# Kernel tuning notes

Hardware: AMD Instinct MI355X
Metric: run time of the kernel (lower is better)

## Reference

```python
import jax, jax.numpy as jnp
import numpy as np

B, S, D = 2, 2048, 2048
HQ, HKV, HD = 16, 8, 128
F = 8192
V = 32000
L = 2
SW = 512
SOFTCAP = 50.0
THETA = 10000.0
EPS = 1e-6
LAYER_TYPES = ("sliding_attention", "full_attention")
SCALE = HD ** -0.5


def _rms_norm(x, w):
    # Gemma-style RMSNorm: fp32 compute, (1 + weight) scale
    x32 = x.astype(jnp.float32)
    n = x32 * jax.lax.rsqrt(jnp.mean(x32 * x32, axis=-1, keepdims=True) + EPS)
    return (n * (1.0 + w.astype(jnp.float32))).astype(x.dtype)


def _rotate_half(x):
    x1, x2 = jnp.split(x, 2, axis=-1)
    return jnp.concatenate([-x2, x1], axis=-1)


def _rope_cos_sin(position_ids):
    inv_freq = 1.0 / (THETA ** (jnp.arange(0, HD, 2, dtype=jnp.float32) / HD))  # [HD/2]
    freqs = position_ids.astype(jnp.float32)[..., None] * inv_freq  # [B,S,HD/2]
    emb = jnp.concatenate([freqs, freqs], axis=-1)  # [B,S,HD]
    return jnp.cos(emb), jnp.sin(emb)


def _apply_rope(q, k, cos, sin):
    # q,k: [B,H,S,HD]; cos,sin: [B,S,HD] -> unsqueeze head dim
    c, s = cos[:, None], sin[:, None]
    return q * c + _rotate_half(q) * s, k * c + _rotate_half(k) * s


def _build_masks(attention_mask, position_ids):
    key_mask = attention_mask.astype(bool)  # [B,S]
    # segment ids from position resets (packed sequences)
    boundaries = (position_ids[:, 1:] <= position_ids[:, :-1]).astype(jnp.int32)
    seg = jnp.cumsum(jnp.concatenate([jnp.ones((B, 1), jnp.int32), boundaries], axis=1), axis=1)
    block = seg[:, :, None] == seg[:, None, :]  # [B,S,S]
    full = (key_mask[:, None, :] & block)[:, None]  # [B,1,S,S]
    rows = jnp.arange(S)
    dist = rows[:, None] - rows[None, :]
    left = (SW + 1) // 2
    right = SW // 2 + 1
    window = ((dist >= 0) & (dist < left)) | ((dist < 0) & (-dist < right))
    sliding = full & window[None, None]
    return {"full_attention": full, "sliding_attention": sliding}


def _attention(x, l, wq, wk, wv, wo, q_norm_w, k_norm_w, cos, sin, mask):
    q = jnp.einsum("bsd,dhe->bhse", x, wq[l].reshape(D, HQ, HD))
    k = jnp.einsum("bsd,dhe->bhse", x, wk[l].reshape(D, HKV, HD))
    v = jnp.einsum("bsd,dhe->bhse", x, wv[l].reshape(D, HKV, HD))
    q = _rms_norm(q, q_norm_w[l])
    k = _rms_norm(k, k_norm_w[l])
    q, k = _apply_rope(q, k, cos, sin)
    rep = HQ // HKV
    k = jnp.repeat(k, rep, axis=1)  # repeat_kv
    v = jnp.repeat(v, rep, axis=1)
    scores = jnp.einsum("bhqd,bhkd->bhqk", q, k) * SCALE
    scores = jnp.tanh(scores / SOFTCAP) * SOFTCAP  # logit softcapping
    big_neg = jnp.finfo(jnp.float32).min
    scores = jnp.where(mask, scores, big_neg)
    probs = jax.nn.softmax(scores.astype(jnp.float32), axis=-1).astype(x.dtype)
    out = jnp.einsum("bhqk,bhkd->bhqd", probs, v)
    out = out.transpose(0, 2, 1, 3).reshape(B, S, HQ * HD)
    return out @ wo[l]


def _mlp(x, l, w_gate_up, w_down):
    gu = x @ w_gate_up[l]
    gate, up = jnp.split(gu, 2, axis=-1)
    return (jax.nn.gelu(gate, approximate=True) * up) @ w_down[l]


def setup_inputs() -> dict:
    key = jax.random.key(0)
    ks = jax.random.split(key, 12)
    w = lambda k, shape: (jax.random.normal(k, shape, jnp.float32) * 0.02)
    inp = {
        "embed": w(ks[0], (V, D)),
        "wq": w(ks[1], (L, D, HQ * HD)),
        "wk": w(ks[2], (L, D, HKV * HD)),
        "wv": w(ks[3], (L, D, HKV * HD)),
        "wo": w(ks[4], (L, HQ * HD, D)),
        "q_norm_w": jnp.zeros((L, HD), jnp.float32),
        "k_norm_w": jnp.zeros((L, HD), jnp.float32),
        "ln_in": jnp.zeros((L, D), jnp.float32),
        "ln_post_attn": jnp.zeros((L, D), jnp.float32),
        "ln_pre_ffn": jnp.zeros((L, D), jnp.float32),
        "ln_post_ffn": jnp.zeros((L, D), jnp.float32),
        "w_gate_up": w(ks[5], (L, D, 2 * F)),
        "w_down": w(ks[6], (L, F, D)),
        "final_norm_w": jnp.zeros((D,), jnp.float32),
        "input_ids": jax.random.randint(ks[7], (B, S), 0, V, jnp.int32),
        "attention_mask": jnp.ones((B, S), jnp.int32),
        # packed sequences: positions reset at the midpoint of each row
        "position_ids": jnp.broadcast_to(
            jnp.concatenate([jnp.arange(S // 2), jnp.arange(S - S // 2)]).astype(jnp.int32)[None, :],
            (B, S),
        ),
    }
    return inp


def reference(embed, wq, wk, wv, wo, q_norm_w, k_norm_w, ln_in, ln_post_attn,
              ln_pre_ffn, ln_post_ffn, w_gate_up, w_down, final_norm_w,
              input_ids, attention_mask, position_ids):
    masks = _build_masks(attention_mask, position_ids)
    cos, sin = _rope_cos_sin(position_ids)
    # scaled word embedding (Gemma style)
    x = embed[input_ids] * jnp.asarray(D ** 0.5, embed.dtype)
    for l in range(L):
        mask = masks[LAYER_TYPES[l]]
        h = _rms_norm(x, ln_in[l])
        h = _attention(h, l, wq, wk, wv, wo, q_norm_w, k_norm_w, cos, sin, mask)
        x = x + _rms_norm(h, ln_post_attn[l])
        h = _rms_norm(x, ln_pre_ffn[l])
        h = _mlp(h, l, w_gate_up, w_down)
        x = x + _rms_norm(h, ln_post_ffn[l])
    return _rms_norm(x, final_norm_w)
```

## Files before the change

kernel.cpp:

```cpp
#include <hip/hip_runtime.h>
#include <cstdint>
#include <cstddef>

typedef __bf16 bf16x8 __attribute__((ext_vector_type(8)));
typedef float  f32x4  __attribute__((ext_vector_type(4)));

#define BATCH 2
#define SEQ   2048
#define DMODEL 2048
#define NHQ   16
#define NHKV  8
#define HDIM  128
#define FFDIM 8192
#define NTOK  4096

__device__ __forceinline__ f32x4 mfma16(bf16x8 a, bf16x8 b, f32x4 c) {
    return __builtin_amdgcn_mfma_f32_16x16x32_bf16(a, b, c, 0, 0, 0);
}

__device__ __forceinline__ void gload16(const __bf16* g, __bf16* l) {
    __builtin_amdgcn_global_load_lds(
        (const __attribute__((address_space(1))) void*)g,
        (__attribute__((address_space(3))) void*)l, 16, 0, 0);
}

__device__ inline float wave_sum64(float v) {
    v += __shfl_xor(v, 1);  v += __shfl_xor(v, 2);  v += __shfl_xor(v, 4);
    v += __shfl_xor(v, 8);  v += __shfl_xor(v, 16); v += __shfl_xor(v, 32);
    return v;
}

__device__ inline float block_sum256(float v, float* lds4) {
    v = wave_sum64(v);
    const int w = threadIdx.x >> 6;
    __syncthreads();
    if ((threadIdx.x & 63) == 0) lds4[w] = v;
    __syncthreads();
    return lds4[0] + lds4[1] + lds4[2] + lds4[3];
}

__device__ __forceinline__ float softcap_exp(float s_raw) {
    const float K1 = 0.08838834764831845f * 0.04f;
    float u = __expf(s_raw * K1);
    return __expf(50.f - 100.f * __builtin_amdgcn_rcpf(1.f + u));
}

__global__ void transpose_cvt(const float* __restrict__ src, __bf16* __restrict__ dst,
                              int K, int N) {
    __shared__ float tile[32][33];
    const int tx = threadIdx.x, ty = threadIdx.y;
    const int n0 = blockIdx.x * 32, k0 = blockIdx.y * 32;
    #pragma unroll
    for (int i = 0; i < 4; ++i)
        tile[ty + i * 8][tx] = src[(size_t)(k0 + ty + i * 8) * N + n0 + tx];
    __syncthreads();
    #pragma unroll
    for (int i = 0; i < 4; ++i)
        dst[(size_t)(n0 + ty + i * 8) * K + k0 + tx] = (__bf16)tile[tx][ty + i * 8];
}

__global__ void transpose_cvt_gu(const float* __restrict__ src, __bf16* __restrict__ dst,
                                 int K, int N) {
    __shared__ float tile[32][33];
    const int tx = threadIdx.x, ty = threadIdx.y;
    const int n0 = blockIdx.x * 32, k0 = blockIdx.y * 32;
    #pragma unroll
    for (int i = 0; i < 4; ++i)
        tile[ty + i * 8][tx] = src[(size_t)(k0 + ty + i * 8) * N + n0 + tx];
    __syncthreads();
    #pragma unroll
    for (int i = 0; i < 4; ++i) {
        int n = n0 + ty + i * 8;
        int rI = (n < 8192) ? (2 * n) : (2 * (n - 8192) + 1);
        dst[(size_t)rI * K + k0 + tx] = (__bf16)tile[tx][ty + i * 8];
    }
}

__global__ void transpose_bf16_k(const __bf16* __restrict__ src0, __bf16* __restrict__ dst0,
                                 int R, int C) {
    __shared__ __bf16 tile[32][34];
    const int z = blockIdx.z;
    const __bf16* src = src0 + (size_t)z * R * C;
    __bf16* dst = dst0 + (size_t)z * R * C;
    const int tx = threadIdx.x, ty = threadIdx.y;
    const int c0 = blockIdx.x * 32, r0 = blockIdx.y * 32;
    #pragma unroll
    for (int i = 0; i < 4; ++i)
        tile[ty + i * 8][tx] = src[(size_t)(r0 + ty + i * 8) * C + c0 + tx];
    __syncthreads();
    #pragma unroll
    for (int i = 0; i < 4; ++i)
        dst[(size_t)(c0 + ty + i * 8) * R + r0 + tx] = tile[tx][ty + i * 8];
}

__global__ __launch_bounds__(256) void embed_k(const float* __restrict__ emb,
                                               const int* __restrict__ ids,
                                               float* __restrict__ x) {
    const int row = blockIdx.x, t = threadIdx.x;
    const int id = ids[row];
    const size_t src = (size_t)id * DMODEL, dst = (size_t)row * DMODEL;
    const float sc = 45.2548339959390f;
    float4 a = *(const float4*)&emb[src + t * 4];
    float4 b = *(const float4*)&emb[src + t * 4 + 1024];
    a.x *= sc; a.y *= sc; a.z *= sc; a.w *= sc;
    b.x *= sc; b.y *= sc; b.z *= sc; b.w *= sc;
    *(float4*)&x[dst + t * 4] = a;
    *(float4*)&x[dst + t * 4 + 1024] = b;
}

__global__ __launch_bounds__(256) void seg_scan(const int* __restrict__ pos,
                                                int* __restrict__ seg) {
    __shared__ int wsum[4];
    const int b = blockIdx.x, t = threadIdx.x;
    const int lane = t & 63, wv = t >> 6;
    const int base = b * SEQ;
    int f[8]; int loc = 0;
    #pragma unroll
    for (int i = 0; i < 8; ++i) {
        int s = t * 8 + i;
        int fl = (s > 0) ? (pos[base + s] <= pos[base + s - 1]) : 0;
        f[i] = fl; loc += fl;
    }
    int sc = loc;
    for (int o = 1; o < 64; o <<= 1) { int n = __shfl_up(sc, o); if (lane >= o) sc += n; }
    if (lane == 63) wsum[wv] = sc;
    __syncthreads();
    int wb = 0;
    for (int i = 0; i < wv; ++i) wb += wsum[i];
    int run = wb + sc - loc + 1;
    #pragma unroll
    for (int i = 0; i < 8; ++i) { run += f[i]; seg[base + t * 8 + i] = run; }
}

template<int MODE, int NH>
__global__ __launch_bounds__(256) void fused_norm_k(
        float* __restrict__ x, const float* __restrict__ hA, const float* __restrict__ hB,
        const float* __restrict__ wA, const float* __restrict__ wB,
        __bf16* __restrict__ outb, float* __restrict__ outf) {
    __shared__ float lds4[4];
    const int row = blockIdx.x, t = threadIdx.x;
    const size_t base = (size_t)row * DMODEL;
    const int c0 = t * 4, c1 = t * 4 + 1024;
    float v[8];
    if constexpr (MODE == 0) {
        float4 a = *(const float4*)&x[base + c0];
        float4 b = *(const float4*)&x[base + c1];
        v[0]=a.x; v[1]=a.y; v[2]=a.z; v[3]=a.w;
        v[4]=b.x; v[5]=b.y; v[6]=b.z; v[7]=b.w;
    } else {
        float4 ha = *(const float4*)&hA[base + c0];
        float4 hb = *(const float4*)&hA[base + c1];
        float hv[8] = {ha.x, ha.y, ha.z, ha.w, hb.x, hb.y, hb.z, hb.w};
        if constexpr (NH == 2) {
            float4 ga = *(const float4*)&hB[base + c0];
            float4 gb = *(const float4*)&hB[base + c1];
            hv[0]+=ga.x; hv[1]+=ga.y; hv[2]+=ga.z; hv[3]+=ga.w;
            hv[4]+=gb.x; hv[5]+=gb.y; hv[6]+=gb.z; hv[7]+=gb.w;
        }
        float ss = 0.f;
        #pragma unroll
        for (int i = 0; i < 8; ++i) ss += hv[i] * hv[i];
        float tot = block_sum256(ss, lds4);
        float rs = rsqrtf(tot * (1.f / DMODEL) + 1e-6f);
        float4 xa = *(const float4*)&x[base + c0];
        float4 xb = *(const float4*)&x[base + c1];
        float xv[8] = {xa.x, xa.y, xa.z, xa.w, xb.x, xb.y, xb.z, xb.w};
        #pragma unroll
        for (int i = 0; i < 8; ++i) {
            int c = (i < 4) ? c0 + i : c1 + i - 4;
            v[i] = xv[i] + hv[i] * rs * (1.f + wA[c]);
        }
        float4 o0 = {v[0], v[1], v[2], v[3]}, o1 = {v[4], v[5], v[6], v[7]};
        *(float4*)&x[base + c0] = o0;
        *(float4*)&x[base + c1] = o1;
    }
    float ss2 = 0.f;
    #pragma unroll
    for (int i = 0; i < 8; ++i) ss2 += v[i] * v[i];
    float tot2 = block_sum256(ss2, lds4);
    float rs2 = rsqrtf(tot2 * (1.f / DMODEL) + 1e-6f);
    #pragma unroll
    for (int i = 0; i < 8; ++i) {
        int c = (i < 4) ? c0 + i : c1 + i - 4;
        float o = v[i] * rs2 * (1.f + wB[c]);
        if constexpr (MODE == 2) outf[base + c] = o;
        else outb[base + c] = (__bf16)o;
    }
}

template<int MH, int NH>
__device__ __forceinline__ void quad(f32x4 (&acc)[8][4], const bf16x8 (&af)[4][2],
                                     const bf16x8 (&bfr)[2][2]) {
    #pragma unroll
    for (int mq = 0; mq < 4; ++mq)
        #pragma unroll
        for (int nq = 0; nq < 2; ++nq)
            #pragma unroll
            for (int ks = 0; ks < 2; ++ks)
                acc[MH*4+mq][NH*2+nq] = mfma16(af[mq][ks], bfr[nq][ks], acc[MH*4+mq][NH*2+nq]);
}

template<typename OutT, int GELU>
__global__ __launch_bounds__(512, 2) void gemm8p(const __bf16* __restrict__ A,
                                                 const __bf16* __restrict__ Bw,
                                                 OutT* __restrict__ C,
                                                 int M, int N, int Ksub, int lda, int ldb) {
    __shared__ __bf16 lds[65536];
    const int z = blockIdx.z;
    A += (size_t)z * Ksub;
    Bw += (size_t)z * Ksub;
    C += (size_t)z * M * N;

    const int nx = gridDim.x;
    const int nwg = nx * gridDim.y;
    const int orig = blockIdx.y * nx + blockIdx.x;
    const int wg = ((nwg & 7) == 0) ? ((orig & 7) * (nwg >> 3) + (orig >> 3)) : orig;
    const int bm = (wg / nx) * 256;
    const int bn = (wg % nx) * 256;

    const int t = threadIdx.x;
    const int w = t >> 6, lane = t & 63;
    const int wm = w >> 2, wn = w & 3;
    const int lg = lane >> 4, lr = lane & 15;

    const int rS = t >> 3, sS = t & 7;
    const int colS = ((sS ^ (rS & 7)) << 3);
    const __bf16* Ag = A + (size_t)(bm + rS) * lda + colS;
    const __bf16* Bg = Bw + (size_t)(bn + rS) * ldb + colS;
    const int nt = Ksub >> 6;

#define STAGE_A(kt, h) { \
        const __bf16* g_ = Ag + (size_t)(h) * 128 * lda + (size_t)(kt) * 64; \
        const int li_ = (((kt) & 1) << 15) + ((h) << 13) + t * 8; \
        gload16(g_, &lds[li_]); \
        gload16(g_ + (size_t)64 * lda, &lds[li_ + 4096]); }
#define STAGE_B(kt, h) { \
        const __bf16* g_ = Bg + (size_t)(h) * 128 * ldb + (size_t)(kt) * 64; \
        const int li_ = (((kt) & 1) << 15) + 16384 + ((h) << 13) + t * 8; \
        gload16(g_, &lds[li_]); \
        gload16(g_ + (size_t)64 * ldb, &lds[li_ + 4096]); }

    f32x4 acc[8][4] = {};
    bf16x8 af[4][2], bf0[2][2], bf1[2][2];

    const int swz = (lr & 7) << 3;
    const int aBase = wm * 8192;
    const int bBase = 16384 + (wn >> 1) * 8192;
    const int bRow0 = (wn & 1) * 64;

    STAGE_A(0, 0); STAGE_A(0, 1); STAGE_B(0, 0); STAGE_B(0, 1);
    if (nt > 1) {
        STAGE_A(1, 0); STAGE_A(1, 1);
        asm volatile("s_waitcnt vmcnt(4)" ::: "memory");
    } else {
        asm volatile("s_waitcnt vmcnt(0)" ::: "memory");
    }
    __builtin_amdgcn_s_barrier();
    asm volatile("" ::: "memory");

    for (int kt = 0; kt < nt; ++kt) {
        const int buf = (kt & 1) << 15;
        const bool p1 = (kt + 1 < nt), p2 = (kt + 2 < nt);
        #pragma unroll
        for (int mq = 0; mq < 4; ++mq)
            #pragma unroll
            for (int ks = 0; ks < 2; ++ks)
                af[mq][ks] = *(const bf16x8*)&lds[buf + aBase + (((mq*16 + lr)*64 + ks*32 + lg*8) ^ swz)];
        #pragma unroll
        for (int nq = 0; nq < 2; ++nq)
            #pragma unroll
            for (int ks = 0; ks < 2; ++ks)
                bf0[nq][ks] = *(const bf16x8*)&lds[buf + bBase + (((bRow0 + nq*16 + lr)*64 + ks*32 + lg*8) ^ swz)];
        __builtin_amdgcn_sched_barrier(0);
        if (p1) STAGE_B(kt + 1, 0);
        __builtin_amdgcn_s_barrier();
        asm volatile("s_waitcnt lgkmcnt(0)" ::: "memory");
        __builtin_amdgcn_sched_barrier(0);
        __builtin_amdgcn_s_setprio(1);
        quad<0,0>(acc, af, bf0);
        __builtin_amdgcn_s_setprio(0);
        __builtin_amdgcn_s_barrier();
        asm volatile("" ::: "memory");
        #pragma unroll
        for (int nq = 0; nq < 2; ++nq)
            #pragma unroll
            for (int ks = 0; ks < 2; ++ks)
                bf1[nq][ks] = *(const bf16x8*)&lds[buf + bBase + (((bRow0 + 32 + nq*16 + lr)*64 + ks*32 + lg*8) ^ swz)];
        __builtin_amdgcn_sched_barrier(0);
        if (p1) STAGE_B(kt + 1, 1);
        __builtin_amdgcn_s_barrier();
        asm volatile("s_waitcnt lgkmcnt(0)" ::: "memory");
        __builtin_amdgcn_sched_barrier(0);
        __builtin_amdgcn_s_setprio(1);
        quad<0,1>(acc, af, bf1);
        __builtin_amdgcn_s_setprio(0);
        __builtin_amdgcn_s_barrier();
        asm volatile("" ::: "memory");
        #pragma unroll
        for (int mq = 0; mq < 4; ++mq)
            #pragma unroll
            for (int ks = 0; ks < 2; ++ks)
                af[mq][ks] = *(const bf16x8*)&lds[buf + aBase + (((64 + mq*16 + lr)*64 + ks*32 + lg*8) ^ swz)];
        __builtin_amdgcn_sched_barrier(0);
        __builtin_amdgcn_s_barrier();
        asm volatile("s_waitcnt lgkmcnt(0)" ::: "memory");
        __builtin_amdgcn_sched_barrier(0);
        __builtin_amdgcn_s_setprio(1);
        quad<1,1>(acc, af, bf1);
        __builtin_amdgcn_s_setprio(0);
        __builtin_amdgcn_s_barrier();
        asm volatile("" ::: "memory");
        if (p2) {
            STAGE_A(kt + 2, 0); STAGE_A(kt + 2, 1);
            asm volatile("s_waitcnt vmcnt(4)" ::: "memory");
        } else if (p1) {
            asm volatile("s_waitcnt vmcnt(0)" ::: "memory");
        }
        __builtin_amdgcn_s_barrier();
        __builtin_amdgcn_sched_barrier(0);
        __builtin_amdgcn_s_setprio(1);
        quad<1,0>(acc, af, bf0);
        __builtin_amdgcn_s_setprio(0);
        __builtin_amdgcn_s_barrier();
        asm volatile("" ::: "memory");
    }
#undef STAGE_A
#undef STAGE_B

    if constexpr (GELU) {
        const int nhalf = N >> 1;
        #pragma unroll
        for (int m = 0; m < 8; ++m)
            #pragma unroll
            for (int n = 0; n < 4; ++n)
                #pragma unroll
                for (int r = 0; r < 4; ++r) {
                    float v = acc[m][n][r];
                    float p = __shfl_xor(v, 1);
                    float a2 = 1.5957691216057308f * (v + 0.044715f * v * v * v);
                    float sig = __builtin_amdgcn_rcpf(1.f + __expf(-a2));
                    float res = v * sig * p;
                    if (!(lane & 1)) {
                        const int row = bm + wm * 128 + m * 16 + lg * 4 + r;
                        const int col = (bn >> 1) + wn * 32 + n * 8 + (lr >> 1);
                        C[(size_t)row * nhalf + col] = (OutT)res;
                    }
                }
    } else {
        #pragma unroll
        for (int m = 0; m < 8; ++m)
            #pragma unroll
            for (int n = 0; n < 4; ++n)
                #pragma unroll
                for (int r = 0; r < 4; ++r) {
                    const int row = bm + wm * 128 + m * 16 + lg * 4 + r;
                    const int col = bn + wn * 64 + n * 16 + lr;
                    C[(size_t)row * N + col] = (OutT)acc[m][n][r];
                }
    }
}

__global__ __launch_bounds__(256) void reduce4(const float* __restrict__ p,
                                               float* __restrict__ out, int n) {
    const int i = (blockIdx.x * 256 + threadIdx.x) * 4;
    float4 a = *(const float4*)&p[i];
    float4 b = *(const float4*)&p[i + n];
    float4 c = *(const float4*)&p[i + 2 * (size_t)n];
    float4 d = *(const float4*)&p[i + 3 * (size_t)n];
    float4 r = {a.x+b.x+c.x+d.x, a.y+b.y+c.y+d.y, a.z+b.z+c.z+d.z, a.w+b.w+c.w+d.w};
    *(float4*)&out[i] = r;
}

__global__ __launch_bounds__(256) void qkv_post(const __bf16* __restrict__ qkv,
                                                const float* __restrict__ qnw,
                                                const float* __restrict__ knw,
                                                const int* __restrict__ posid,
                                                __bf16* __restrict__ qg,
                                                __bf16* __restrict__ kg,
                                                __bf16* __restrict__ vg) {
    const int slot = blockIdx.x * 4 + (threadIdx.x >> 6);
    const int lane = threadIdx.x & 63;
    const int token = slot >> 5, j = slot & 31;
    const int b = token >> 11, s = token & (SEQ - 1);
    int base;
    const float* nw = nullptr;
    if (j < 16)      { base = j * 128;                nw = qnw; }
    else if (j < 24) { base = 2048 + (j - 16) * 128;  nw = knw; }
    else             { base = 3072 + (j - 24) * 128; }
    float e0 = (float)qkv[(size_t)token * 4096 + base + lane];
    float e1 = (float)qkv[(size_t)token * 4096 + base + lane + 64];
    if (j < 24) {
        float ss = wave_sum64(e0 * e0 + e1 * e1);
        float rs = rsqrtf(ss * (1.f / 128.f) + 1e-6f);
        e0 *= rs * (1.f + nw[lane]);
        e1 *= rs * (1.f + nw[lane + 64]);
        float p = (float)posid[token];
        float inv = exp2f(-13.287712379549449f * ((float)lane * (1.f / 64.f)));
        float f = p * inv;
        float c = cosf(f), sn = sinf(f);
        float o0 = e0 * c - e1 * sn;
        float o1 = e1 * c + e0 * sn;
        e0 = o0; e1 = o1;
    }
    size_t dst; __bf16* out;
    if (j < 16)      { dst = ((size_t)(b * NHQ  + j)        * SEQ + s) * HDIM; out = qg; }
    else if (j < 24) { dst = ((size_t)(b * NHKV + (j - 16)) * SEQ + s) * HDIM; out = kg; }
    else             { dst = ((size_t)(b * NHKV + (j - 24)) * SEQ + s) * HDIM; out = vg; }
    out[dst + lane] = (__bf16)e0;
    out[dst + lane + 64] = (__bf16)e1;
}

template<int SLIDING>
__global__ __launch_bounds__(256, 2) void attn_k(const __bf16* __restrict__ qg,
                                                 const __bf16* __restrict__ kg,
                                                 const __bf16* __restrict__ vtg,
                                                 const int* __restrict__ seg,
                                                 const int* __restrict__ amask,
                                                 __bf16* __restrict__ outg) {
    __shared__ __align__(16) __bf16 Ks[64][136];
    __shared__ __align__(16) __bf16 Vs[128][72];
    __shared__ __align__(16) __bf16 Ps[4][16][72];
    __shared__ int segq_s[64], segk_s[64], kmk_s[64];
    __shared__ int flag_s;
    const int bh = blockIdx.y;
    const int b = bh >> 4, h = bh & 15, kvh = h >> 1;
    const int qb = blockIdx.x * 64;
    const int t = threadIdx.x, w = t >> 6, lane = t & 63;
    const int lg = lane >> 4, lr = lane & 15;
    const int segbase = b * SEQ;

    const size_t qoff = ((size_t)(b * NHQ + h) * SEQ + qb + w * 16) * HDIM;
    bf16x8 qf[4];
    #pragma unroll
    for (int kk = 0; kk < 4; ++kk)
        qf[kk] = *(const bf16x8*)&qg[qoff + (size_t)lr * HDIM + kk * 32 + lg * 8];
    if (t < 64) segq_s[t] = seg[segbase + qb + t];

    const int sqmin = seg[segbase + qb], sqmax = seg[segbase + qb + 63];

    const int krow = t >> 4, kcol = (t & 15) * 8;
    const int vrow = t >> 3, vcol = (t & 7) * 8;
    const __bf16* kB = kg + ((size_t)(b * NHKV + kvh) * SEQ) * HDIM + (size_t)krow * HDIM + kcol;
    const __bf16* vB = vtg + ((size_t)(b * NHKV + kvh) * HDIM + vrow) * SEQ + vcol;

    auto chunk_active = [&](int kb) -> bool {
        if (SLIDING && (qb - kb < -318 || qb - kb > 319)) return false;
        int skmin = seg[segbase + kb], skmax = seg[segbase + kb + 63];
        return (skmax >= sqmin) && (skmin <= sqmax);
    };
    auto next_kb = [&](int kb) -> int {
        for (kb += 64; kb < SEQ; kb += 64)
            if (chunk_active(kb)) return kb;
        return SEQ;
    };

    int4 kr0, kr1, kr2, kr3, vr0, vr1, vr2, vr3;
#define LOADR(kb_) { \
        kr0 = *(const int4*)(kB + (size_t)(kb_) * HDIM); \
        kr1 = *(const int4*)(kB + (size_t)((kb_) + 16) * HDIM); \
        kr2 = *(const int4*)(kB + (size_t)((kb_) + 32) * HDIM); \
        kr3 = *(const int4*)(kB + (size_t)((kb_) + 48) * HDIM); \
        vr0 = *(const int4*)(vB + (kb_)); \
        vr1 = *(const int4*)(vB + (size_t)32 * SEQ + (kb_)); \
        vr2 = *(const int4*)(vB + (size_t)64 * SEQ + (kb_)); \
        vr3 = *(const int4*)(vB + (size_t)96 * SEQ + (kb_)); }

    f32x4 oacc[8] = {};
    float den[4] = {0.f, 0.f, 0.f, 0.f};

    int kb = chunk_active(0) ? 0 : next_kb(0);
    if (kb < SEQ) LOADR(kb);

    while (kb < SEQ) {
        const int nkb = next_kb(kb);
        __syncthreads();
        *(int4*)&Ks[krow     ][kcol] = kr0;
        *(int4*)&Ks[krow + 16][kcol] = kr1;
        *(int4*)&Ks[krow + 32][kcol] = kr2;
        *(int4*)&Ks[krow + 48][kcol] = kr3;
        *(int4*)&Vs[vrow     ][vcol] = vr0;
        *(int4*)&Vs[vrow + 32][vcol] = vr1;
        *(int4*)&Vs[vrow + 64][vcol] = vr2;
        *(int4*)&Vs[vrow + 96][vcol] = vr3;
        if (w == 0) {
            int m = amask[segbase + kb + lane];
            int sk = seg[segbase + kb + lane];
            kmk_s[lane] = m; segk_s[lane] = sk;
            bool allm = (__ballot(m != 0) == ~0ull);
            bool segu = __all(sk == sqmin) && (sqmin == sqmax);
            bool wall = !SLIDING || (qb - kb >= -193 && qb - kb <= 192);
            if (lane == 0) flag_s = (allm && segu && wall) ? 1 : 0;
        }
        __syncthreads();
        if (nkb < SEQ) LOADR(nkb);
        const bool fast = (flag_s != 0);

        #pragma unroll
        for (int n = 0; n < 4; ++n) {
            f32x4 sc = {};
            #pragma unroll
            for (int kk = 0; kk < 4; ++kk) {
                bf16x8 bfr = *(const bf16x8*)&Ks[n * 16 + lr][kk * 32 + lg * 8];
                sc = mfma16(qf[kk], bfr, sc);
            }
            if (fast) {
                #pragma unroll
                for (int r = 0; r < 4; ++r) {
                    int row = lg * 4 + r;
                    float p = softcap_exp(sc[r]);
                    den[r] += p;
                    Ps[w][row][n * 16 + lr] = (__bf16)p;
                }
            } else {
                #pragma unroll
                for (int r = 0; r < 4; ++r) {
                    int row = lg * 4 + r;
                    int qi = qb + w * 16 + row;
                    int ki = kb + n * 16 + lr;
                    bool ok = (kmk_s[n * 16 + lr] != 0) &&
                              (segq_s[w * 16 + row] == segk_s[n * 16 + lr]);
                    if (SLIDING) { int d = qi - ki; ok = ok && (d >= -256) && (d <= 255); }
                    float p = ok ? softcap_exp(sc[r]) : 0.f;
                    den[r] += p;
                    Ps[w][row][n * 16 + lr] = (__bf16)p;
                }
            }
        }
        #pragma unroll
        for (int kk2 = 0; kk2 < 2; ++kk2) {
            bf16x8 pf = *(const bf16x8*)&Ps[w][lr][kk2 * 32 + lg * 8];
            #pragma unroll
            for (int n2 = 0; n2 < 8; ++n2) {
                bf16x8 vf = *(const bf16x8*)&Vs[n2 * 16 + lr][kk2 * 32 + lg * 8];
                oacc[n2] = mfma16(pf, vf, oacc[n2]);
            }
        }
        kb = nkb;
    }
#undef LOADR
    #pragma unroll
    for (int r = 0; r < 4; ++r) {
        float v = den[r];
        v += __shfl_xor(v, 1); v += __shfl_xor(v, 2);
        v += __shfl_xor(v, 4); v += __shfl_xor(v, 8);
        den[r] = __builtin_amdgcn_rcpf(v);
    }
    #pragma unroll
    for (int n2 = 0; n2 < 8; ++n2)
        #pragma unroll
        for (int r = 0; r < 4; ++r) {
            int row = qb + w * 16 + lg * 4 + r;
            float val = oacc[n2][r] * den[r];
            outg[((size_t)(b * SEQ) + row) * DMODEL + h * HDIM + n2 * 16 + lr] = (__bf16)val;
        }
}

extern "C" void kernel_launch(void* const* d_in, const int* in_sizes, int n_in,
                              void* d_out, int out_size, void* d_ws, size_t ws_size,
                              hipStream_t stream) {
    const float* embedw = (const float*)d_in[0];
    const float* wq   = (const float*)d_in[1];
    const float* wk   = (const float*)d_in[2];
    const float* wv   = (const float*)d_in[3];
    const float* wo   = (const float*)d_in[4];
    const float* qnw  = (const float*)d_in[5];
    const float* knw  = (const float*)d_in[6];
    const float* lnin = (const float*)d_in[7];
    const float* lnpa = (const float*)d_in[8];
    const float* lnpf = (const float*)d_in[9];
    const float* lnpff= (const float*)d_in[10];
    const float* wguW = (const float*)d_in[11];
    const float* wdnW = (const float*)d_in[12];
    const float* fnw  = (const float*)d_in[13];
    const int* ids    = (const int*)d_in[14];
    const int* amask  = (const int*)d_in[15];
    const int* posid  = (const int*)d_in[16];
    float* outp = (float*)d_out;

    char* ws = (char*)d_ws;
    size_t off = 0;
    auto A = [&](size_t b) -> char* {
        char* p = ws + off;
        off = (off + b + 255) & ~(size_t)255;
        return p;
    };
    __bf16* qkvwt = (__bf16*)A((size_t)4096 * 2048 * 2);
    __bf16* wot   = (__bf16*)A((size_t)2048 * 2048 * 2);
    __bf16* wgut  = (__bf16*)A((size_t)16384 * 2048 * 2);
    __bf16* wdnt  = (__bf16*)A((size_t)2048 * 8192 * 2);
    float*  x     = (float*)A((size_t)NTOK * DMODEL * 4);
    __bf16* hbuf  = (__bf16*)A((size_t)NTOK * DMODEL * 2);
    __bf16* qkvb  = (__bf16*)A((size_t)NTOK * 4096 * 2);
    __bf16* qbh   = (__bf16*)A((size_t)BATCH * NHQ  * SEQ * HDIM * 2);
    __bf16* kbh   = (__bf16*)A((size_t)BATCH * NHKV * SEQ * HDIM * 2);
    __bf16* vbh   = (__bf16*)A((size_t)BATCH * NHKV * SEQ * HDIM * 2);
    __bf16* vtbh  = (__bf16*)A((size_t)BATCH * NHKV * SEQ * HDIM * 2);
    __bf16* attnb = (__bf16*)A((size_t)NTOK * DMODEL * 2);
    float*  h2    = (float*)A((size_t)NTOK * DMODEL * 4);
    __bf16* actb  = (__bf16*)A((size_t)2048 * FFDIM * 2);
    float*  pbuf  = (float*)A((size_t)4 * 2048 * 2048 * 4);
    int*    seg   = (int*)A((size_t)BATCH * SEQ * 4);
    if (off > ws_size) return;

    const dim3 tb(32, 8);
    seg_scan<<<BATCH, 256, 0, stream>>>(posid, seg);
    embed_k<<<NTOK, 256, 0, stream>>>(embedw, ids, x);
    fused_norm_k<0,1><<<NTOK, 256, 0, stream>>>(x, nullptr, nullptr, nullptr, lnin, hbuf, nullptr);

    for (int l = 0; l < 2; ++l) {
        transpose_cvt<<<dim3(64, 64), tb, 0, stream>>>(wq + (size_t)l * 2048 * 2048,
            qkvwt, 2048, 2048);
        transpose_cvt<<<dim3(32, 64), tb, 0, stream>>>(wk + (size_t)l * 2048 * 1024,
            qkvwt + (size_t)2048 * 2048, 2048, 1024);
        transpose_cvt<<<dim3(32, 64), tb, 0, stream>>>(wv + (size_t)l * 2048 * 1024,
            qkvwt + (size_t)3072 * 2048, 2048, 1024);
        transpose_cvt<<<dim3(64, 64), tb, 0, stream>>>(wo + (size_t)l * 2048 * 2048,
            wot, 2048, 2048);
        transpose_cvt_gu<<<dim3(512, 64), tb, 0, stream>>>(wguW + (size_t)l * 2048 * 16384,
            wgut, 2048, 16384);
        transpose_cvt<<<dim3(64, 256), tb, 0, stream>>>(wdnW + (size_t)l * 8192 * 2048,
            wdnt, 8192, 2048);

        gemm8p<__bf16,0><<<dim3(16, 16, 1), 512, 0, stream>>>(hbuf, qkvwt, qkvb,
                                                              4096, 4096, 2048, 2048, 2048);
        qkv_post<<<32768, 256, 0, stream>>>(qkvb, qnw + l * 128, knw + l * 128, posid,
                                            qbh, kbh, vbh);
        transpose_bf16_k<<<dim3(4, 64, BATCH * NHKV), tb, 0, stream>>>(vbh, vtbh, SEQ, HDIM);
        if (l == 0)
            attn_k<1><<<dim3(SEQ / 64, BATCH * NHQ), 256, 0, stream>>>(qbh, kbh, vtbh, seg,
                                                                       amask, attnb);
        else
            attn_k<0><<<dim3(SEQ / 64, BATCH * NHQ), 256, 0, stream>>>(qbh, kbh, vtbh, seg,
                                                                       amask, attnb);
        gemm8p<float,0><<<dim3(8, 16, 2), 512, 0, stream>>>(attnb, wot, pbuf,
                                                            4096, 2048, 1024, 2048, 2048);
        fused_norm_k<1,2><<<NTOK, 256, 0, stream>>>(x, pbuf, pbuf + (size_t)4096 * 2048,
                                                    lnpa + l * 2048, lnpf + l * 2048,
                                                    hbuf, nullptr);
        for (int c = 0; c < 2; ++c) {
            gemm8p<__bf16,1><<<dim3(64, 8, 1), 512, 0, stream>>>(
                hbuf + (size_t)c * 2048 * 2048, wgut, actb, 2048, 16384, 2048, 2048, 2048);
            gemm8p<float,0><<<dim3(8, 8, 4), 512, 0, stream>>>(actb, wdnt, pbuf,
                                                               2048, 2048, 2048, 8192, 8192);
            reduce4<<<4096, 256, 0, stream>>>(pbuf, h2 + (size_t)c * 2048 * 2048, 2048 * 2048);
        }
        if (l == 0)
            fused_norm_k<1,1><<<NTOK, 256, 0, stream>>>(x, h2, nullptr, lnpff, lnin + 2048,
                                                        hbuf, nullptr);
        else
            fused_norm_k<2,1><<<NTOK, 256, 0, stream>>>(x, h2, nullptr, lnpff + 2048, fnw,
                                                        nullptr, outp);
    }
}
```

Before: 1.604 ms.

## Run MLP GEMMs over all tokens at once and fold split-K reduce into norm

The MLP used to run in two token chunks of 2048, each with a 4-way split-K down projection followed by a separate reduce kernel. It now runs as one gate/up GEMM over all 4096 tokens and a 2-way split-K down GEMM, and the two partial sums are added inside the fused norm kernel. The separate reduce pass and h2 buffer go away. The GEMM tile ordering also changes to a grouped-M swizzle for better L2 reuse. In exchange the activation buffer must be twice as large, and fused_norm_k<2,2> has to be a valid template instantiation.

```diff
diff --git a/kernel.cpp b/kernel.cpp
--- a/kernel.cpp
+++ b/kernel.cpp
@@ -212,11 +212,17 @@
     C += (size_t)z * M * N;
 
     const int nx = gridDim.x;
-    const int nwg = nx * gridDim.y;
+    const int ny = gridDim.y;
+    const int nwg = nx * ny;
     const int orig = blockIdx.y * nx + blockIdx.x;
     const int wg = ((nwg & 7) == 0) ? ((orig & 7) * (nwg >> 3) + (orig >> 3)) : orig;
-    const int bm = (wg / nx) * 256;
-    const int bn = (wg % nx) * 256;
+    const int gsize = 8 * nx;
+    const int gid = wg / gsize;
+    const int first_m = gid * 8;
+    const int rows = min(8, ny - first_m);
+    const int loc = wg - gid * gsize;
+    const int bm = (first_m + loc % rows) * 256;
+    const int bn = (loc / rows) * 256;
 
     const int t = threadIdx.x;
     const int w = t >> 6, lane = t & 63;
@@ -358,17 +364,6 @@
                     C[(size_t)row * N + col] = (OutT)acc[m][n][r];
                 }
     }
-}
-
-__global__ __launch_bounds__(256) void reduce4(const float* __restrict__ p,
-                                               float* __restrict__ out, int n) {
-    const int i = (blockIdx.x * 256 + threadIdx.x) * 4;
-    float4 a = *(const float4*)&p[i];
-    float4 b = *(const float4*)&p[i + n];
-    float4 c = *(const float4*)&p[i + 2 * (size_t)n];
-    float4 d = *(const float4*)&p[i + 3 * (size_t)n];
-    float4 r = {a.x+b.x+c.x+d.x, a.y+b.y+c.y+d.y, a.z+b.z+c.z+d.z, a.w+b.w+c.w+d.w};
-    *(float4*)&out[i] = r;
 }
 
 __global__ __launch_bounds__(256) void qkv_post(const __bf16* __restrict__ qkv,
@@ -596,9 +591,8 @@
     __bf16* vbh   = (__bf16*)A((size_t)BATCH * NHKV * SEQ * HDIM * 2);
     __bf16* vtbh  = (__bf16*)A((size_t)BATCH * NHKV * SEQ * HDIM * 2);
     __bf16* attnb = (__bf16*)A((size_t)NTOK * DMODEL * 2);
-    float*  h2    = (float*)A((size_t)NTOK * DMODEL * 4);
-    __bf16* actb  = (__bf16*)A((size_t)2048 * FFDIM * 2);
-    float*  pbuf  = (float*)A((size_t)4 * 2048 * 2048 * 4);
+    __bf16* actb  = (__bf16*)A((size_t)NTOK * FFDIM * 2);
+    float*  pbuf  = (float*)A((size_t)2 * NTOK * DMODEL * 4);
     int*    seg   = (int*)A((size_t)BATCH * SEQ * 4);
     if (off > ws_size) return;
 
@@ -634,21 +628,18 @@
                                                                        amask, attnb);
         gemm8p<float,0><<<dim3(8, 16, 2), 512, 0, stream>>>(attnb, wot, pbuf,
                                                             4096, 2048, 1024, 2048, 2048);
-        fused_norm_k<1,2><<<NTOK, 256, 0, stream>>>(x, pbuf, pbuf + (size_t)4096 * 2048,
+        fused_norm_k<1,2><<<NTOK, 256, 0, stream>>>(x, pbuf, pbuf + (size_t)NTOK * DMODEL,
                                                     lnpa + l * 2048, lnpf + l * 2048,
                                                     hbuf, nullptr);
-        for (int c = 0; c < 2; ++c) {
-            gemm8p<__bf16,1><<<dim3(64, 8, 1), 512, 0, stream>>>(
-                hbuf + (size_t)c * 2048 * 2048, wgut, actb, 2048, 16384, 2048, 2048, 2048);
-            gemm8p<float,0><<<dim3(8, 8, 4), 512, 0, stream>>>(actb, wdnt, pbuf,
-                                                               2048, 2048, 2048, 8192, 8192);
-            reduce4<<<4096, 256, 0, stream>>>(pbuf, h2 + (size_t)c * 2048 * 2048, 2048 * 2048);
-        }
+        gemm8p<__bf16,1><<<dim3(64, 16, 1), 512, 0, stream>>>(hbuf, wgut, actb,
+                                                              4096, 16384, 2048, 2048, 2048);
+        gemm8p<float,0><<<dim3(8, 16, 2), 512, 0, stream>>>(actb, wdnt, pbuf,
+                                                            4096, 2048, 4096, 8192, 8192);
         if (l == 0)
-            fused_norm_k<1,1><<<NTOK, 256, 0, stream>>>(x, h2, nullptr, lnpff, lnin + 2048,
-                                                        hbuf, nullptr);
+            fused_norm_k<1,2><<<NTOK, 256, 0, stream>>>(x, pbuf, pbuf + (size_t)NTOK * DMODEL,
+                                                        lnpff, lnin + 2048, hbuf, nullptr);
         else
-            fused_norm_k<2,1><<<NTOK, 256, 0, stream>>>(x, h2, nullptr, lnpff + 2048, fnw,
-                                                        nullptr, outp);
-    }
-}
+            fused_norm_k<2,2><<<NTOK, 256, 0, stream>>>(x, pbuf, pbuf + (size_t)NTOK * DMODEL,
+                                                        lnpff + 2048, fnw, nullptr, outp);
+    }
+}
```

Result: faster. 1.511 ms (-5.8%).
